# Performance work log

Measured on AMD Instinct MI355X. Metric: run time of the kernel, lower is better.

Reference implementation:

```python
import jax, jax.numpy as jnp
import numpy as np

N = 100000
IN_DIM = 256
OUT_DIM = 256
E = 3200000
SLOPE = 0.2


def setup_inputs() -> dict:
    key = jax.random.key(0)
    ks = jax.random.split(key, 14)
    xav = lambda k, shape: jax.random.normal(k, shape, jnp.float32) * np.sqrt(2.0 / sum(shape))
    inp = {
        "H": jax.random.normal(ks[0], (N, IN_DIM), jnp.float32),
        "W0": xav(ks[1], (IN_DIM, OUT_DIM)),
        "W1": xav(ks[2], (IN_DIM, OUT_DIM)),
        "W2": xav(ks[3], (IN_DIM, OUT_DIM)),
        "a0": xav(ks[4], (2 * OUT_DIM,)),
        "a1": xav(ks[5], (2 * OUT_DIM,)),
        "a2": xav(ks[6], (2 * OUT_DIM,)),
        "bias": jnp.zeros((OUT_DIM,), jnp.float32),
    }
    for i, r in enumerate(["0", "1", "2"]):
        inp["row" + r] = jax.random.randint(ks[7 + 2 * i], (E,), 0, N, jnp.int32)
        inp["col" + r] = jax.random.randint(ks[8 + 2 * i], (E,), 0, N, jnp.int32)
    return inp


def _gat_type(H, W, a, row, col):
    # Wh: [N, out_dim]
    Wh = H @ W
    # attention logits per edge: leaky_relu(a_dst . Wh[row] + a_src . Wh[col])
    s_dst = Wh @ a[:OUT_DIM]   # [N]
    s_src = Wh @ a[OUT_DIM:]   # [N]
    e = jax.nn.leaky_relu(s_dst[row] + s_src[col], SLOPE)  # [E]
    # segment softmax over destination node (row)
    e_max = jax.ops.segment_max(e, row, num_segments=N)    # [N]
    e_shifted = jnp.exp(e - e_max[row])
    e_sum = jax.ops.segment_sum(e_shifted, row, num_segments=N)
    alpha = e_shifted / jnp.maximum(e_sum[row], 1e-12)     # [E]
    # weighted aggregation of source features into destinations
    return jax.ops.segment_sum(alpha[:, None] * Wh[col], row, num_segments=N)


def reference(H, row0, col0, row1, col1, row2, col2, W0, W1, W2, a0, a1, a2, bias):
    out = _gat_type(H, W0, a0, row0, col0)
    out = out + _gat_type(H, W1, a1, row1, col1)
    out = out + _gat_type(H, W2, a2, row2, col2)
    return out + bias
```

## Files before the change

kernel.cpp:

```cpp
#include <hip/hip_runtime.h>
#include <cstdint>
#include <cstddef>

#define DIM 256
#define SLOPE 0.2f
#define BSHIFT 8
#define SLOTS 9216
#define TILE 4096

typedef __attribute__((ext_vector_type(8))) short short8;
typedef __attribute__((ext_vector_type(4))) float f32x4;

__device__ __forceinline__ unsigned short f2bf(float f) {
  unsigned u = __float_as_uint(f);
  u += 0x7fffu + ((u >> 16) & 1u);
  return (unsigned short)(u >> 16);
}
__device__ __forceinline__ float bf2f(unsigned short h) {
  return __uint_as_float(((unsigned)h) << 16);
}

__global__ void wtrans_kernel(const float* __restrict__ W0, const float* __restrict__ W1,
                              const float* __restrict__ W2, unsigned short* __restrict__ Wt) {
  const float* W = blockIdx.y == 0 ? W0 : (blockIdx.y == 1 ? W1 : W2);
  int k = blockIdx.x, n = threadIdx.x;
  Wt[((size_t)blockIdx.y * DIM + n) * DIM + k] = f2bf(W[k * DIM + n]);
}

__global__ __launch_bounds__(256, 2) void gemm3_scores_kernel(
    const float* __restrict__ H, const unsigned short* __restrict__ Wt,
    const float* __restrict__ a0, const float* __restrict__ a1,
    const float* __restrict__ a2, unsigned short* __restrict__ Whb,
    float* __restrict__ s_dst, float* __restrict__ s_src, int N, size_t wstride) {
  __shared__ unsigned short Hs[64][264];
  __shared__ unsigned short Os[4][16][264];
  const int t = threadIdx.x;
  const int r0 = blockIdx.x * 64;
#pragma unroll
  for (int i = 0; i < 16; ++i) {
    int idx = t + i * 256;
    int row = idx >> 6;
    int c4 = idx & 63;
    int r = r0 + row;
    float4 h = (r < N) ? *(const float4*)&H[(size_t)r * DIM + c4 * 4]
                       : make_float4(0.f, 0.f, 0.f, 0.f);
    unsigned lo = (unsigned)f2bf(h.x) | ((unsigned)f2bf(h.y) << 16);
    unsigned hi = (unsigned)f2bf(h.z) | ((unsigned)f2bf(h.w) << 16);
    *(uint2*)&Hs[row][c4 * 4] = make_uint2(lo, hi);
  }
  __syncthreads();
  const int wave = t >> 6, lane = t & 63;
  const int q = lane >> 4, m = lane & 15;
  const int rowbase = wave * 16;
  short8 Af[8];
#pragma unroll
  for (int k0 = 0; k0 < 8; ++k0)
    Af[k0] = *(const short8*)&Hs[rowbase + m][k0 * 32 + q * 8];
  const float* aptr[3] = {a0, a1, a2};
#pragma unroll
  for (int ty = 0; ty < 3; ++ty) {
    const unsigned short* Wtt = Wt + (size_t)ty * DIM * DIM;
    const float* a = aptr[ty];
    f32x4 acc[16];
#pragma unroll
    for (int j = 0; j < 16; ++j) acc[j] = (f32x4){0.f, 0.f, 0.f, 0.f};
#pragma unroll
    for (int k0 = 0; k0 < 8; ++k0) {
#pragma unroll
      for (int j = 0; j < 16; ++j) {
        short8 Bf = *(const short8*)&Wtt[(size_t)(j * 16 + m) * DIM + k0 * 32 + q * 8];
        acc[j] = __builtin_amdgcn_mfma_f32_16x16x32_bf16(Af[k0], Bf, acc[j], 0, 0, 0);
      }
    }
    float pd[4] = {0, 0, 0, 0}, ps[4] = {0, 0, 0, 0};
#pragma unroll
    for (int j = 0; j < 16; ++j) {
      int col = j * 16 + m;
      float ad = a[col], as = a[DIM + col];
#pragma unroll
      for (int reg = 0; reg < 4; ++reg) {
        float v = acc[j][reg];
        pd[reg] += v * ad;
        ps[reg] += v * as;
        Os[wave][q * 4 + reg][col] = f2bf(v);
      }
    }
#pragma unroll
    for (int off = 8; off >= 1; off >>= 1) {
#pragma unroll
      for (int reg = 0; reg < 4; ++reg) {
        pd[reg] += __shfl_down(pd[reg], off);
        ps[reg] += __shfl_down(ps[reg], off);
      }
    }
    if (m == 0) {
#pragma unroll
      for (int reg = 0; reg < 4; ++reg) {
        int r = r0 + rowbase + q * 4 + reg;
        if (r < N) {
          s_dst[(size_t)ty * N + r] = pd[reg];
          s_src[(size_t)ty * N + r] = ps[reg];
        }
      }
    }
    unsigned short* wout = Whb + (size_t)ty * wstride;
#pragma unroll
    for (int row = 0; row < 16; ++row) {
      int r = r0 + rowbase + row;
      if (r < N)
        *(uint2*)&wout[(size_t)r * DIM + lane * 4] = *(const uint2*)&Os[wave][row][lane * 4];
    }
  }
}

__global__ __launch_bounds__(256, 2) void gemm_scores_kernel(
    const float* __restrict__ H, const unsigned short* __restrict__ Wt,
    const float* __restrict__ a, unsigned short* __restrict__ Whb,
    float* __restrict__ s_dst, float* __restrict__ s_src, int N) {
  __shared__ unsigned short Hs[64][264];
  __shared__ unsigned short Os[4][16][264];
  const int t = threadIdx.x;
  const int r0 = blockIdx.x * 64;
#pragma unroll
  for (int i = 0; i < 16; ++i) {
    int idx = t + i * 256;
    int row = idx >> 6;
    int c4 = idx & 63;
    int r = r0 + row;
    float4 h = (r < N) ? *(const float4*)&H[(size_t)r * DIM + c4 * 4]
                       : make_float4(0.f, 0.f, 0.f, 0.f);
    unsigned lo = (unsigned)f2bf(h.x) | ((unsigned)f2bf(h.y) << 16);
    unsigned hi = (unsigned)f2bf(h.z) | ((unsigned)f2bf(h.w) << 16);
    *(uint2*)&Hs[row][c4 * 4] = make_uint2(lo, hi);
  }
  __syncthreads();
  const int wave = t >> 6, lane = t & 63;
  const int q = lane >> 4, m = lane & 15;
  const int rowbase = wave * 16;
  short8 Af[8];
#pragma unroll
  for (int k0 = 0; k0 < 8; ++k0)
    Af[k0] = *(const short8*)&Hs[rowbase + m][k0 * 32 + q * 8];
  f32x4 acc[16];
#pragma unroll
  for (int j = 0; j < 16; ++j) acc[j] = (f32x4){0.f, 0.f, 0.f, 0.f};
#pragma unroll
  for (int k0 = 0; k0 < 8; ++k0) {
#pragma unroll
    for (int j = 0; j < 16; ++j) {
      short8 Bf = *(const short8*)&Wt[(size_t)(j * 16 + m) * DIM + k0 * 32 + q * 8];
      acc[j] = __builtin_amdgcn_mfma_f32_16x16x32_bf16(Af[k0], Bf, acc[j], 0, 0, 0);
    }
  }
  float pd[4] = {0, 0, 0, 0}, ps[4] = {0, 0, 0, 0};
#pragma unroll
  for (int j = 0; j < 16; ++j) {
    int col = j * 16 + m;
    float ad = a[col], as = a[DIM + col];
#pragma unroll
    for (int reg = 0; reg < 4; ++reg) {
      float v = acc[j][reg];
      pd[reg] += v * ad;
      ps[reg] += v * as;
      Os[wave][q * 4 + reg][col] = f2bf(v);
    }
  }
#pragma unroll
  for (int off = 8; off >= 1; off >>= 1) {
#pragma unroll
    for (int reg = 0; reg < 4; ++reg) {
      pd[reg] += __shfl_down(pd[reg], off);
      ps[reg] += __shfl_down(ps[reg], off);
    }
  }
  if (m == 0) {
#pragma unroll
    for (int reg = 0; reg < 4; ++reg) {
      int r = r0 + rowbase + q * 4 + reg;
      if (r < N) {
        s_dst[r] = pd[reg];
        s_src[r] = ps[reg];
      }
    }
  }
  __syncthreads();
#pragma unroll
  for (int row = 0; row < 16; ++row) {
    int r = r0 + rowbase + row;
    if (r < N)
      *(uint2*)&Whb[(size_t)r * DIM + lane * 4] = *(const uint2*)&Os[wave][row][lane * 4];
  }
}

__global__ __launch_bounds__(256) void bin_edges_kernel(
    const int* __restrict__ r0, const int* __restrict__ r1, const int* __restrict__ r2,
    const int* __restrict__ c0, const int* __restrict__ c1, const int* __restrict__ c2,
    int* __restrict__ bcnt,
    unsigned* __restrict__ pairs,
    int E, int NB) {
  __shared__ int hist[512];
  __shared__ int curs[512];
  const int ty = blockIdx.y;
  const int* rr = ty == 0 ? r0 : (ty == 1 ? r1 : r2);
  const int* cc = ty == 0 ? c0 : (ty == 1 ? c1 : c2);
  const int t = threadIdx.x;
  const int base = blockIdx.x * TILE;
  for (int i = t; i < NB; i += 256) hist[i] = 0;
  __syncthreads();
  int rows[TILE / 256];
#pragma unroll
  for (int i = 0; i < TILE / 256; ++i) {
    int e = base + t + i * 256;
    int r = (e < E) ? rr[e] : -1;
    rows[i] = r;
    if (r >= 0) atomicAdd(&hist[r >> BSHIFT], 1);
  }
  __syncthreads();
  for (int b = t; b < NB; b += 256) {
    int h = hist[b];
    int off = h ? atomicAdd(&bcnt[ty * NB + b], h) : 0;
    curs[b] = b * SLOTS + off;
  }
  __syncthreads();
  unsigned* pt = pairs + (size_t)ty * NB * SLOTS;
#pragma unroll
  for (int i = 0; i < TILE / 256; ++i) {
    int e = base + t + i * 256;
    if (e >= E) continue;
    int r = rows[i];
    int b = r >> BSHIFT;
    int pos = atomicAdd(&curs[b], 1);
    if (pos - b * SLOTS < SLOTS)
      pt[pos] = ((unsigned)(r & 255) << 17) | (unsigned)cc[e];
  }
}

__global__ __launch_bounds__(256) void bucket_sort_kernel(
    const int* __restrict__ bcnt, unsigned* __restrict__ pairs,
    int* __restrict__ rp, int* __restrict__ deg, int N, int NB) {
  __shared__ int hist[256];
  __shared__ int excl[256];
  __shared__ int curs[256];
  __shared__ unsigned stage[SLOTS];
  const int b = blockIdx.x, ty = blockIdx.y;
  const int t = threadIdx.x;
  int cnt = bcnt[ty * NB + b];
  if (cnt > SLOTS) cnt = SLOTS;
  unsigned* pb = pairs + (size_t)ty * NB * SLOTS + (size_t)b * SLOTS;
  hist[t] = 0;
  __syncthreads();
  for (int i = t; i < cnt; i += 256) atomicAdd(&hist[pb[i] >> 17], 1);
  __syncthreads();
  int v = hist[t];
  excl[t] = v;
  __syncthreads();
  for (int off = 1; off < 256; off <<= 1) {
    int u = (t >= off) ? excl[t - off] : 0;
    __syncthreads();
    excl[t] += u;
    __syncthreads();
  }
  int ex = excl[t] - v;
  curs[t] = ex;
  int r = (b << BSHIFT) + t;
  if (r < N) {
    rp[(size_t)ty * N + r] = b * SLOTS + ex;
    deg[(size_t)ty * N + r] = v;
  }
  __syncthreads();
  for (int i = t; i < cnt; i += 256) {
    unsigned p = pb[i];
    int pos = atomicAdd(&curs[p >> 17], 1);
    stage[pos] = p;
  }
  __syncthreads();
  for (int i = t; i < cnt; i += 256) pb[i] = stage[i];
}

__global__ __launch_bounds__(256) void gat_fused_kernel(
    const int* __restrict__ rp, const int* __restrict__ deg,
    const unsigned* __restrict__ pairs,
    const float* __restrict__ s_dst, const float* __restrict__ s_src,
    const unsigned short* __restrict__ Whb,
    const float* __restrict__ bias, float* __restrict__ out, int N, int NB,
    size_t wstride) {
  __shared__ uint2 ebuf[4][64];
  int n = (int)((blockIdx.x * (unsigned)blockDim.x + threadIdx.x) >> 6);
  if (n >= N) return;
  const int wid = (threadIdx.x >> 6);
  const int lane = threadIdx.x & 63;
  float4 total = {0.f, 0.f, 0.f, 0.f};
  for (int t = 0; t < 3; ++t) {
    int beg = rp[(size_t)t * N + n], d = deg[(size_t)t * N + n];
    if (d == 0) continue;
    int end = beg + d;
    const unsigned* pcol = pairs + (size_t)t * NB * SLOTS;
    const float* ss = s_src + (size_t)t * N;
    float sd = s_dst[(size_t)t * N + n];
    const unsigned short* wbase = Whb + (size_t)t * wstride + lane * 4;
    float mx = -__builtin_inff();
    for (int p = beg + lane; p < end; p += 64) {
      float v = sd + ss[pcol[p] & 0x1FFFFu];
      v = v > 0.f ? v : SLOPE * v;
      mx = fmaxf(mx, v);
    }
#pragma unroll
    for (int off = 32; off >= 1; off >>= 1) mx = fmaxf(mx, __shfl_down(mx, off));
    mx = __shfl(mx, 0);
    float4 acc = {0.f, 0.f, 0.f, 0.f};
    float psum = 0.f;
    for (int base = beg; base < end; base += 64) {
      int myp = base + lane;
      int cnt = end - base;
      if (cnt > 64) cnt = 64;
      unsigned myc = 0;
      float mype = 0.f;
      if (myp < end) {
        myc = pcol[myp] & 0x1FFFFu;
        float v = sd + ss[myc];
        v = v > 0.f ? v : SLOPE * v;
        mype = __expf(v - mx);
      }
      psum += mype;
      ebuf[wid][lane] = make_uint2(myc, __float_as_uint(mype));
#pragma unroll 8
      for (int j = 0; j < cnt; ++j) {
        uint2 cp = ebuf[wid][j];
        float pe = __uint_as_float(cp.y);
        ushort4 w = *(const ushort4*)&wbase[(size_t)cp.x * DIM];
        acc.x += pe * bf2f(w.x);
        acc.y += pe * bf2f(w.y);
        acc.z += pe * bf2f(w.z);
        acc.w += pe * bf2f(w.w);
      }
    }
#pragma unroll
    for (int off = 32; off >= 1; off >>= 1) psum += __shfl_down(psum, off);
    psum = __shfl(psum, 0);
    float inv = 1.f / fmaxf(psum, 1e-12f);
    total.x += acc.x * inv;
    total.y += acc.y * inv;
    total.z += acc.z * inv;
    total.w += acc.w * inv;
  }
  float4 cur = ((const float4*)bias)[lane];
  cur.x += total.x;
  cur.y += total.y;
  cur.z += total.z;
  cur.w += total.w;
  *((float4*)(out + (size_t)n * DIM) + lane) = cur;
}

__global__ __launch_bounds__(256) void gat_node_kernel(
    const int* __restrict__ rp, const int* __restrict__ deg,
    const unsigned* __restrict__ pcol,
    const float* __restrict__ s_dst, const float* __restrict__ s_src,
    const unsigned short* __restrict__ Whb,
    const float* __restrict__ bias, float* __restrict__ out, int N, int first) {
  __shared__ uint2 ebuf[4][64];
  int n = (int)((blockIdx.x * (unsigned)blockDim.x + threadIdx.x) >> 6);
  if (n >= N) return;
  const int wid = (threadIdx.x >> 6);
  const int lane = threadIdx.x & 63;
  int beg = rp[n], d = deg[n], end = beg + d;
  if (!first && d == 0) return;
  float sd = s_dst[n];
  float mx = -__builtin_inff();
  for (int p = beg + lane; p < end; p += 64) {
    float v = sd + s_src[pcol[p] & 0x1FFFFu];
    v = v > 0.f ? v : SLOPE * v;
    mx = fmaxf(mx, v);
  }
#pragma unroll
  for (int off = 32; off >= 1; off >>= 1) mx = fmaxf(mx, __shfl_down(mx, off));
  mx = __shfl(mx, 0);
  const unsigned short* wbase = Whb + lane * 4;
  float4 acc = {0.f, 0.f, 0.f, 0.f};
  float psum = 0.f;
  for (int base = beg; base < end; base += 64) {
    int myp = base + lane;
    int cnt = end - base;
    if (cnt > 64) cnt = 64;
    unsigned myc = 0;
    float mype = 0.f;
    if (myp < end) {
      myc = pcol[myp] & 0x1FFFFu;
      float v = sd + s_src[myc];
      v = v > 0.f ? v : SLOPE * v;
      mype = __expf(v - mx);
    }
    psum += mype;
    ebuf[wid][lane] = make_uint2(myc, __float_as_uint(mype));
#pragma unroll 8
    for (int j = 0; j < cnt; ++j) {
      uint2 cp = ebuf[wid][j];
      float pe = __uint_as_float(cp.y);
      ushort4 w = *(const ushort4*)&wbase[(size_t)cp.x * DIM];
      acc.x += pe * bf2f(w.x);
      acc.y += pe * bf2f(w.y);
      acc.z += pe * bf2f(w.z);
      acc.w += pe * bf2f(w.w);
    }
  }
#pragma unroll
  for (int off = 32; off >= 1; off >>= 1) psum += __shfl_down(psum, off);
  psum = __shfl(psum, 0);
  float inv = 1.f / fmaxf(psum, 1e-12f);
  float4* o = (float4*)(out + (size_t)n * DIM) + lane;
  float4 cur = first ? ((const float4*)bias)[lane] : *o;
  cur.x += acc.x * inv;
  cur.y += acc.y * inv;
  cur.z += acc.z * inv;
  cur.w += acc.w * inv;
  *o = cur;
}

static inline size_t align256(size_t x) { return (x + 255) & ~(size_t)255; }

extern "C" void kernel_launch(void* const* d_in, const int* in_sizes, int n_in,
                              void* d_out, int out_size, void* d_ws, size_t ws_size,
                              hipStream_t stream) {
  const float* H = (const float*)d_in[0];
  const float* W[3] = {(const float*)d_in[1], (const float*)d_in[2], (const float*)d_in[3]};
  const float* a[3] = {(const float*)d_in[4], (const float*)d_in[5], (const float*)d_in[6]};
  const float* bias = (const float*)d_in[7];
  const int* row[3] = {(const int*)d_in[8], (const int*)d_in[10], (const int*)d_in[12]};
  const int* col[3] = {(const int*)d_in[9], (const int*)d_in[11], (const int*)d_in[13]};
  const int N = in_sizes[0] / DIM;
  const int E = in_sizes[8];
  const int NB = (N + 255) >> BSHIFT;
  float* out = (float*)d_out;

  char* ws = (char*)d_ws;
  size_t off = 0;
  unsigned short* Wt = (unsigned short*)(ws + off);
  off = align256(off + (size_t)3 * DIM * DIM * sizeof(unsigned short));
  float* s_dst = (float*)(ws + off);
  off = align256(off + (size_t)3 * N * sizeof(float));
  float* s_src = (float*)(ws + off);
  off = align256(off + (size_t)3 * N * sizeof(float));
  int* bcnt = (int*)(ws + off);
  off = align256(off + (size_t)3 * NB * sizeof(int));
  int* rp = (int*)(ws + off);
  off = align256(off + (size_t)3 * N * sizeof(int));
  int* deg = (int*)(ws + off);
  off = align256(off + (size_t)3 * N * sizeof(int));
  unsigned* pairs = (unsigned*)(ws + off);
  off = align256(off + (size_t)3 * NB * SLOTS * sizeof(unsigned));
  unsigned short* Whb = (unsigned short*)(ws + off);
  const size_t whb_bytes = align256((size_t)N * DIM * sizeof(unsigned short));
  const size_t wstride = whb_bytes / sizeof(unsigned short);
  const int fused = (ws_size >= off + 3 * whb_bytes) ? 1 : 0;

  wtrans_kernel<<<dim3(DIM, 3), 256, 0, stream>>>(W[0], W[1], W[2], Wt);
  hipMemsetAsync(bcnt, 0, (size_t)3 * NB * sizeof(int), stream);
  const int eb = (E + TILE - 1) / TILE;
  bin_edges_kernel<<<dim3(eb, 3), 256, 0, stream>>>(row[0], row[1], row[2], col[0], col[1],
                                                    col[2], bcnt, pairs, E, NB);
  bucket_sort_kernel<<<dim3(NB, 3), 256, 0, stream>>>(bcnt, pairs, rp, deg, N, NB);

  const int gemm_blocks = (N + 63) / 64;
  const int gat_blocks = (N * 64 + 255) / 256;
  if (fused) {
    gemm3_scores_kernel<<<gemm_blocks, 256, 0, stream>>>(H, Wt, a[0], a[1], a[2], Whb, s_dst,
                                                         s_src, N, wstride);
    gat_fused_kernel<<<gat_blocks, 256, 0, stream>>>(rp, deg, pairs, s_dst, s_src, Whb, bias,
                                                     out, N, NB, wstride);
  } else {
    for (int t = 0; t < 3; ++t) {
      gemm_scores_kernel<<<gemm_blocks, 256, 0, stream>>>(H, Wt + (size_t)t * DIM * DIM, a[t],
                                                          Whb, s_dst + (size_t)t * N,
                                                          s_src + (size_t)t * N, N);
      gat_node_kernel<<<gat_blocks, 256, 0, stream>>>(
          rp + (size_t)t * N, deg + (size_t)t * N, pairs + (size_t)t * NB * SLOTS,
          s_dst + (size_t)t * N, s_src + (size_t)t * N, Whb, bias, out, N, t == 0 ? 1 : 0);
    }
  }
  (void)n_in;
  (void)out_size;
  (void)ws_size;
}
```

Before: 1.532 ms.

## Double rows per wave in fused GEMM to reuse W fragments across two tiles

The fused three-type GEMM+score kernel now processes 128 rows per block, and each wave computes two 16-row MFMA tiles that share every loaded W fragment. This halves the global/L2 reads of W per row computed. The output staging buffer is shrunk to a 4-row slice per wave and written in quarter-wave phases, keeping LDS use roughly constant despite the larger H tile. The cost is doubled accumulator registers (128 floats), which may lower occupancy or cause spills under launch_bounds(256,2). The ty loop is also no longer unrolled.

```diff
diff --git a/kernel.cpp b/kernel.cpp
--- a/kernel.cpp
+++ b/kernel.cpp
@@ -32,12 +32,12 @@
     const float* __restrict__ a0, const float* __restrict__ a1,
     const float* __restrict__ a2, unsigned short* __restrict__ Whb,
     float* __restrict__ s_dst, float* __restrict__ s_src, int N, size_t wstride) {
-  __shared__ unsigned short Hs[64][264];
-  __shared__ unsigned short Os[4][16][264];
+  __shared__ unsigned short Hs[128][264];
+  __shared__ unsigned short Os[4][4][264];
   const int t = threadIdx.x;
-  const int r0 = blockIdx.x * 64;
-#pragma unroll
-  for (int i = 0; i < 16; ++i) {
+  const int r0 = blockIdx.x * 128;
+#pragma unroll
+  for (int i = 0; i < 32; ++i) {
     int idx = t + i * 256;
     int row = idx >> 6;
     int c4 = idx & 63;
@@ -51,64 +51,92 @@
   __syncthreads();
   const int wave = t >> 6, lane = t & 63;
   const int q = lane >> 4, m = lane & 15;
-  const int rowbase = wave * 16;
-  short8 Af[8];
-#pragma unroll
-  for (int k0 = 0; k0 < 8; ++k0)
-    Af[k0] = *(const short8*)&Hs[rowbase + m][k0 * 32 + q * 8];
+  const int rowbase = wave * 32;
+  short8 Af0[8], Af1[8];
+#pragma unroll
+  for (int k0 = 0; k0 < 8; ++k0) {
+    Af0[k0] = *(const short8*)&Hs[rowbase + m][k0 * 32 + q * 8];
+    Af1[k0] = *(const short8*)&Hs[rowbase + 16 + m][k0 * 32 + q * 8];
+  }
   const float* aptr[3] = {a0, a1, a2};
-#pragma unroll
   for (int ty = 0; ty < 3; ++ty) {
     const unsigned short* Wtt = Wt + (size_t)ty * DIM * DIM;
     const float* a = aptr[ty];
-    f32x4 acc[16];
-#pragma unroll
-    for (int j = 0; j < 16; ++j) acc[j] = (f32x4){0.f, 0.f, 0.f, 0.f};
+    f32x4 acc0[16], acc1[16];
+#pragma unroll
+    for (int j = 0; j < 16; ++j) {
+      acc0[j] = (f32x4){0.f, 0.f, 0.f, 0.f};
+      acc1[j] = (f32x4){0.f, 0.f, 0.f, 0.f};
+    }
 #pragma unroll
     for (int k0 = 0; k0 < 8; ++k0) {
 #pragma unroll
       for (int j = 0; j < 16; ++j) {
         short8 Bf = *(const short8*)&Wtt[(size_t)(j * 16 + m) * DIM + k0 * 32 + q * 8];
-        acc[j] = __builtin_amdgcn_mfma_f32_16x16x32_bf16(Af[k0], Bf, acc[j], 0, 0, 0);
-      }
-    }
-    float pd[4] = {0, 0, 0, 0}, ps[4] = {0, 0, 0, 0};
+        acc0[j] = __builtin_amdgcn_mfma_f32_16x16x32_bf16(Af0[k0], Bf, acc0[j], 0, 0, 0);
+        acc1[j] = __builtin_amdgcn_mfma_f32_16x16x32_bf16(Af1[k0], Bf, acc1[j], 0, 0, 0);
+      }
+    }
+    float pd0[4] = {0, 0, 0, 0}, ps0[4] = {0, 0, 0, 0};
+    float pd1[4] = {0, 0, 0, 0}, ps1[4] = {0, 0, 0, 0};
 #pragma unroll
     for (int j = 0; j < 16; ++j) {
       int col = j * 16 + m;
       float ad = a[col], as = a[DIM + col];
 #pragma unroll
       for (int reg = 0; reg < 4; ++reg) {
-        float v = acc[j][reg];
-        pd[reg] += v * ad;
-        ps[reg] += v * as;
-        Os[wave][q * 4 + reg][col] = f2bf(v);
+        float v0 = acc0[j][reg], v1 = acc1[j][reg];
+        pd0[reg] += v0 * ad;
+        ps0[reg] += v0 * as;
+        pd1[reg] += v1 * ad;
+        ps1[reg] += v1 * as;
       }
     }
 #pragma unroll
     for (int off = 8; off >= 1; off >>= 1) {
 #pragma unroll
       for (int reg = 0; reg < 4; ++reg) {
-        pd[reg] += __shfl_down(pd[reg], off);
-        ps[reg] += __shfl_down(ps[reg], off);
+        pd0[reg] += __shfl_down(pd0[reg], off);
+        ps0[reg] += __shfl_down(ps0[reg], off);
+        pd1[reg] += __shfl_down(pd1[reg], off);
+        ps1[reg] += __shfl_down(ps1[reg], off);
       }
     }
     if (m == 0) {
 #pragma unroll
       for (int reg = 0; reg < 4; ++reg) {
-        int r = r0 + rowbase + q * 4 + reg;
-        if (r < N) {
-          s_dst[(size_t)ty * N + r] = pd[reg];
-          s_src[(size_t)ty * N + r] = ps[reg];
+        int ra = r0 + rowbase + q * 4 + reg;
+        int rb = ra + 16;
+        if (ra < N) {
+          s_dst[(size_t)ty * N + ra] = pd0[reg];
+          s_src[(size_t)ty * N + ra] = ps0[reg];
         }
+        if (rb < N) {
+          s_dst[(size_t)ty * N + rb] = pd1[reg];
+          s_src[(size_t)ty * N + rb] = ps1[reg];
+        }
       }
     }
     unsigned short* wout = Whb + (size_t)ty * wstride;
 #pragma unroll
-    for (int row = 0; row < 16; ++row) {
-      int r = r0 + rowbase + row;
-      if (r < N)
-        *(uint2*)&wout[(size_t)r * DIM + lane * 4] = *(const uint2*)&Os[wave][row][lane * 4];
+    for (int g = 0; g < 2; ++g) {
+#pragma unroll
+      for (int p = 0; p < 4; ++p) {
+        if (q == p) {
+#pragma unroll
+          for (int j = 0; j < 16; ++j)
+#pragma unroll
+            for (int reg = 0; reg < 4; ++reg)
+              Os[wave][reg][j * 16 + m] = f2bf(g ? acc1[j][reg] : acc0[j][reg]);
+        }
+#pragma unroll
+        for (int rr = 0; rr < 4; ++rr) {
+          int r = r0 + rowbase + g * 16 + p * 4 + rr;
+          if (r < N)
+            *(uint2*)&wout[(size_t)r * DIM + lane * 4] =
+                *(const uint2*)&Os[wave][rr][lane * 4];
+        }
+      }
     }
   }
 }
@@ -459,18 +487,17 @@
                                                     col[2], bcnt, pairs, E, NB);
   bucket_sort_kernel<<<dim3(NB, 3), 256, 0, stream>>>(bcnt, pairs, rp, deg, N, NB);
 
-  const int gemm_blocks = (N + 63) / 64;
   const int gat_blocks = (N * 64 + 255) / 256;
   if (fused) {
-    gemm3_scores_kernel<<<gemm_blocks, 256, 0, stream>>>(H, Wt, a[0], a[1], a[2], Whb, s_dst,
-                                                         s_src, N, wstride);
+    gemm3_scores_kernel<<<(N + 127) / 128, 256, 0, stream>>>(H, Wt, a[0], a[1], a[2], Whb,
+                                                             s_dst, s_src, N, wstride);
     gat_fused_kernel<<<gat_blocks, 256, 0, stream>>>(rp, deg, pairs, s_dst, s_src, Whb, bias,
                                                      out, N, NB, wstride);
   } else {
     for (int t = 0; t < 3; ++t) {
-      gemm_scores_kernel<<<gemm_blocks, 256, 0, stream>>>(H, Wt + (size_t)t * DIM * DIM, a[t],
-                                                          Whb, s_dst + (size_t)t * N,
-                                                          s_src + (size_t)t * N, N);
+      gemm_scores_kernel<<<(N + 63) / 64, 256, 0, stream>>>(H, Wt + (size_t)t * DIM * DIM,
+                                                            a[t], Whb, s_dst + (size_t)t * N,
+                                                            s_src + (size_t)t * N, N);
       gat_node_kernel<<<gat_blocks, 256, 0, stream>>>(
           rp + (size_t)t * N, deg + (size_t)t * N, pairs + (size_t)t * NB * SLOTS,
           s_dst + (size_t)t * N, s_src + (size_t)t * N, Whb, bias, out, N, t == 0 ? 1 : 0);
```

Measured after the change: 1.426 ms. 6.9% less time.
